# Performance work log

Hardware: AMD Instinct MI355X
Metric: run time of the kernel (lower is better)

## Reference

```python
import jax, jax.numpy as jnp
import numpy as np

N_NODES = 50000
N_EDGES = 640000
IN_CH = 64
EDGE_DIM = 16
HID = 128
OUT = 128
L = 5
N_GRAPHS = 128
BN_EPS = 1e-5


def setup_inputs() -> dict:
    key = jax.random.key(0)
    ks = jax.random.split(key, 16)

    def w(k, shape, fan_in):
        return jax.random.normal(k, shape, jnp.float32) / np.sqrt(fan_in)

    inp = {}
    inp["x"] = jax.random.normal(ks[0], (N_NODES, IN_CH), jnp.float32)
    inp["edge_index"] = jax.random.randint(ks[1], (2, N_EDGES), 0, N_NODES)
    inp["edge_attr"] = jax.random.normal(ks[2], (N_EDGES, EDGE_DIM), jnp.float32)
    inp["batch"] = jnp.sort(jax.random.randint(ks[3], (N_NODES,), 0, N_GRAPHS))
    # node / edge encoders
    inp["node_w"] = w(ks[4], (IN_CH, HID), IN_CH)
    inp["node_b"] = jnp.zeros((HID,), jnp.float32)
    inp["edge_w"] = w(ks[5], (EDGE_DIM, HID), EDGE_DIM)
    inp["edge_b"] = jnp.zeros((HID,), jnp.float32)
    # per-layer GINEConv params (stacked over L layers)
    inp["eps"] = jnp.zeros((L,), jnp.float32)  # train_eps init 0
    inp["lin_w"] = w(ks[6], (L, HID, HID), HID)       # GINEConv internal edge lin
    inp["lin_b"] = jnp.zeros((L, HID), jnp.float32)
    inp["mlp1_w"] = w(ks[7], (L, HID, 2 * HID), HID)
    inp["mlp1_b"] = jnp.zeros((L, 2 * HID), jnp.float32)
    inp["mlp2_w"] = w(ks[8], (L, 2 * HID, HID), 2 * HID)
    inp["mlp2_b"] = jnp.zeros((L, HID), jnp.float32)
    inp["bn_g"] = jnp.ones((L, HID), jnp.float32)
    inp["bn_b"] = jnp.zeros((L, HID), jnp.float32)
    # output MLP: HID -> HID//2 -> OUT
    inp["out_w1"] = w(ks[9], (HID, HID // 2), HID)
    inp["out_b1"] = jnp.zeros((HID // 2,), jnp.float32)
    inp["out_w2"] = w(ks[10], (HID // 2, OUT), HID // 2)
    inp["out_b2"] = jnp.zeros((OUT,), jnp.float32)
    return inp


def reference(x, edge_index, edge_attr, batch, node_w, node_b, edge_w, edge_b,
              eps, lin_w, lin_b, mlp1_w, mlp1_b, mlp2_w, mlp2_b, bn_g, bn_b,
              out_w1, out_b1, out_w2, out_b2):
    n_nodes = x.shape[0]
    src, dst = edge_index[0], edge_index[1]
    # node / edge encoders (dropout is identity in eval)
    h = jax.nn.relu(x @ node_w + node_b)            # [N, H]
    e = edge_attr @ edge_w + edge_b                  # [E, H]
    n_layers = lin_w.shape[0]
    for l in range(n_layers):
        # GINEConv: message = relu(x_src + lin(edge_emb)); aggregate = scatter-sum to dst
        m = jax.nn.relu(h[src] + e @ lin_w[l] + lin_b[l])      # [E, H]
        agg = jax.ops.segment_sum(m, dst, num_segments=n_nodes)  # [N, H]
        z = (1.0 + eps[l]) * h + agg
        # GINE MLP: H -> 2H -> H
        z = jax.nn.relu(z @ mlp1_w[l] + mlp1_b[l]) @ mlp2_w[l] + mlp2_b[l]
        # BatchNorm over nodes (training-mode batch statistics)
        mu = z.mean(axis=0)
        var = z.var(axis=0)
        z = (z - mu) * jax.lax.rsqrt(var + BN_EPS) * bn_g[l] + bn_b[l]
        # residual then relu
        h = jax.nn.relu(z + h)
    # global mean pool per graph
    counts = jax.ops.segment_sum(jnp.ones((n_nodes,), h.dtype), batch, num_segments=N_GRAPHS)
    pooled = jax.ops.segment_sum(h, batch, num_segments=N_GRAPHS) / jnp.maximum(counts, 1.0)[:, None]
    # output MLP (dropout identity in eval)
    logits = jax.nn.relu(pooled @ out_w1 + out_b1) @ out_w2 + out_b2
    return (logits, pooled)
```

## Files before the change

### kernel.cpp

```cpp
#include <hip/hip_runtime.h>

#define N_NODES  50000
#define NPAD     50048
#define N_EDGES  640000
#define IN_CH    64
#define EDGE_DIM 16
#define HID      128
#define HID2     256
#define NLAYER   5
#define NGRAPH   128
#define MT64     (NPAD / 64)

typedef unsigned short ushort_t;
typedef __attribute__((ext_vector_type(8))) short short8;
typedef __attribute__((ext_vector_type(4))) short s16x4;
typedef __attribute__((ext_vector_type(4))) float f32x4;
typedef __attribute__((ext_vector_type(2))) float f32x2;

__device__ __forceinline__ float b2f(ushort_t u) {
    union { unsigned v; float f; } x; x.v = ((unsigned)u) << 16; return x.f;
}
__device__ __forceinline__ ushort_t f2b(float f) {
    union { float f; unsigned u; } x; x.f = f;
    unsigned u = x.u;
    unsigned r = (u + 0x7FFFu + ((u >> 16) & 1u)) >> 16;
    return (ushort_t)r;
}

__global__ void k_transpose_cvt(const float* __restrict__ src, ushort_t* __restrict__ dst,
                                int B, int K, int Nn) {
    long total = (long)B * K * Nn;
    for (long i = (long)blockIdx.x * blockDim.x + threadIdx.x; i < total;
         i += (long)gridDim.x * blockDim.x) {
        int b = (int)(i / ((long)K * Nn));
        int rem = (int)(i - (long)b * K * Nn);
        int k = rem / Nn;
        int n = rem - k * Nn;
        dst[(long)b * K * Nn + (long)n * K + k] = f2b(src[i]);
    }
}

__global__ __launch_bounds__(128) void k_combine(const float* __restrict__ ew,
                                                 const float* __restrict__ eb,
                                                 const float* __restrict__ lw,
                                                 const float* __restrict__ lb,
                                                 ushort_t* __restrict__ WcbT,
                                                 float* __restrict__ cc) {
    int l = blockIdx.x, j = threadIdx.x;
    float accW[EDGE_DIM];
#pragma unroll
    for (int k = 0; k < EDGE_DIM; ++k) accW[k] = 0.f;
    float accc = 0.f;
    for (int i = 0; i < HID; ++i) {
        float lwv = lw[((long)l * HID + i) * HID + j];
        accc = fmaf(eb[i], lwv, accc);
#pragma unroll
        for (int k = 0; k < EDGE_DIM; ++k)
            accW[k] = fmaf(ew[k * HID + i], lwv, accW[k]);
    }
    ushort_t* wp = WcbT + ((long)l * HID + j) * 32;
#pragma unroll
    for (int k = 0; k < EDGE_DIM; ++k) wp[k] = f2b(accW[k]);
#pragma unroll
    for (int k = EDGE_DIM; k < 32; ++k) wp[k] = 0;
    cc[l * HID + j] = accc + lb[l * HID + j];
}

__global__ __launch_bounds__(256) void k_hist(const int* __restrict__ ei, int* __restrict__ deg) {
    int e = blockIdx.x * 256 + threadIdx.x;
    if (e < N_EDGES) atomicAdd(&deg[ei[N_EDGES + e]], 1);
}

__global__ __launch_bounds__(1024) void k_scan1(const int* __restrict__ deg,
                                                int* __restrict__ offs, int* __restrict__ bsum) {
    __shared__ int s[1024];
    int i = blockIdx.x * 1024 + threadIdx.x;
    int v = (i < N_NODES) ? deg[i] : 0;
    s[threadIdx.x] = v;
    __syncthreads();
    for (int off = 1; off < 1024; off <<= 1) {
        int t = (threadIdx.x >= off) ? s[threadIdx.x - off] : 0;
        __syncthreads();
        s[threadIdx.x] += t;
        __syncthreads();
    }
    if (i < N_NODES) offs[i] = s[threadIdx.x] - v;
    if (threadIdx.x == 1023) bsum[blockIdx.x] = s[1023];
}

__global__ void k_scan2(int* __restrict__ bsum, int nb) {
    if (threadIdx.x == 0 && blockIdx.x == 0) {
        int acc = 0;
        for (int i = 0; i < nb; ++i) { int v = bsum[i]; bsum[i] = acc; acc += v; }
    }
}

__global__ __launch_bounds__(1024) void k_scan3(int* __restrict__ offs, const int* __restrict__ bsum) {
    int i = blockIdx.x * 1024 + threadIdx.x;
    if (i < N_NODES) offs[i] += bsum[blockIdx.x];
}

__global__ __launch_bounds__(256) void k_scatter1(const int* __restrict__ ei,
                                                  const int* __restrict__ offs,
                                                  int* __restrict__ cursor,
                                                  int* __restrict__ perm) {
    int e = blockIdx.x * 256 + threadIdx.x;
    if (e >= N_EDGES) return;
    int d = ei[N_EDGES + e];
    int pos = offs[d] + atomicAdd(&cursor[d], 1);
    perm[pos] = e;
}

__global__ __launch_bounds__(256) void k_gather(const int* __restrict__ perm,
                                                const int* __restrict__ ei,
                                                const float* __restrict__ ea,
                                                int* __restrict__ src_s,
                                                ushort_t* __restrict__ ea_sb) {
    int p = blockIdx.x * 256 + threadIdx.x;
    if (p >= N_EDGES) return;
    int e = perm[p];
    src_s[p] = ei[e];
    const f32x4* srcp = (const f32x4*)(ea + (long)e * EDGE_DIM);
    f32x4 v0 = srcp[0], v1 = srcp[1], v2 = srcp[2], v3 = srcp[3];
    short8 o0, o1;
#pragma unroll
    for (int j = 0; j < 4; ++j) {
        o0[j] = (short)f2b(v0[j]); o0[4 + j] = (short)f2b(v1[j]);
        o1[j] = (short)f2b(v2[j]); o1[4 + j] = (short)f2b(v3[j]);
    }
    short8* dst = (short8*)(ea_sb + (long)p * EDGE_DIM);
    dst[0] = o0;
    dst[1] = o1;
}

__global__ __launch_bounds__(256) void k_node_enc(const float* __restrict__ x,
                                                  const ushort_t* __restrict__ w0T,
                                                  const float* __restrict__ nb,
                                                  float* __restrict__ h,
                                                  ushort_t* __restrict__ hb) {
    __shared__ __align__(16) short lB[HID * IN_CH];
    for (int c = threadIdx.x; c < HID * IN_CH / 8; c += 256) {
        int row = c >> 3, k0 = (c & 7) * 8;
        short8 v = *(const short8*)(w0T + row * IN_CH + k0);
        int g = (k0 >> 3) ^ (row & 7);
        *(short8*)&lB[row * IN_CH + g * 8] = v;
    }
    __syncthreads();
    int wv = threadIdx.x >> 6, l6 = threadIdx.x & 63;
    int lr = l6 & 15, lg = l6 >> 4;
    int grow = blockIdx.x * 64 + wv * 16 + lr;
    f32x4 acc[8];
#pragma unroll
    for (int nt = 0; nt < 8; ++nt) acc[nt] = (f32x4){0.f, 0.f, 0.f, 0.f};
#pragma unroll
    for (int kt = 0; kt < 2; ++kt) {
        int kk = kt * 32 + lg * 8;
        short8 a = {0, 0, 0, 0, 0, 0, 0, 0};
        if (grow < N_NODES) {
            const float* xr = x + (long)grow * IN_CH + kk;
            f32x4 v0 = *(const f32x4*)xr;
            f32x4 v1 = *(const f32x4*)(xr + 4);
#pragma unroll
            for (int j = 0; j < 4; ++j) { a[j] = (short)f2b(v0[j]); a[4 + j] = (short)f2b(v1[j]); }
        }
#pragma unroll
        for (int nt = 0; nt < 8; ++nt) {
            int brow = nt * 16 + lr;
            short8 b = *(const short8*)&lB[brow * IN_CH + (((kk >> 3) ^ (brow & 7)) << 3)];
            acc[nt] = __builtin_amdgcn_mfma_f32_16x16x32_bf16(a, b, acc[nt], 0, 0, 0);
        }
    }
    int orow0 = blockIdx.x * 64 + wv * 16 + lg * 4;
#pragma unroll
    for (int nt = 0; nt < 8; ++nt) {
        int col = nt * 16 + lr;
        float bias = nb[col];
#pragma unroll
        for (int r = 0; r < 4; ++r) {
            int row = orow0 + r;
            if (row < N_NODES) {
                float v = fmaxf(acc[nt][r] + bias, 0.f);
                h[(long)row * HID + col] = v;
                hb[(long)row * HID + col] = f2b(v);
            }
        }
    }
}

__global__ __launch_bounds__(256) void k_edgegemm(const ushort_t* __restrict__ ea_sb,
                                                  const ushort_t* __restrict__ WcbT,
                                                  const float* __restrict__ cc,
                                                  ushort_t* __restrict__ g, int l,
                                                  int ce0, int ce1) {
    int wv = threadIdx.x >> 6, l6 = threadIdx.x & 63;
    int lr = l6 & 15, lg = l6 >> 4;
    short8 af[8];
    f32x4 cv[8];
    const ushort_t* wp = WcbT + (long)l * HID * 32;
#pragma unroll
    for (int nt = 0; nt < 8; ++nt) {
        af[nt] = *(const short8*)(wp + (nt * 16 + lr) * 32 + lg * 8);
        cv[nt] = *(const f32x4*)(cc + l * HID + nt * 16 + lg * 4);
    }
    for (int it = 0; it < 4; ++it) {
        int e0 = ce0 + blockIdx.x * 256 + wv * 64 + it * 16;
        int e = e0 + lr;
        short8 b = {0, 0, 0, 0, 0, 0, 0, 0};
        if (e < ce1 && lg < 2) b = *(const short8*)(ea_sb + (long)e * EDGE_DIM + lg * 8);
        f32x4 acc[8];
#pragma unroll
        for (int nt = 0; nt < 8; ++nt) acc[nt] = (f32x4){0.f, 0.f, 0.f, 0.f};
#pragma unroll
        for (int nt = 0; nt < 8; ++nt)
            acc[nt] = __builtin_amdgcn_mfma_f32_16x16x32_bf16(af[nt], b, acc[nt], 0, 0, 0);
        if (e < ce1) {
            ushort_t* gp = g + (long)(e - ce0) * HID + lg * 4;
#pragma unroll
            for (int nt = 0; nt < 8; ++nt) {
                s16x4 o;
#pragma unroll
                for (int r = 0; r < 4; ++r) o[r] = (short)f2b(acc[nt][r] + cv[nt][r]);
                *(s16x4*)(gp + nt * 16) = o;
            }
        }
    }
}

__global__ __launch_bounds__(256) void k_edge2(const ushort_t* __restrict__ g,
                                               const int* __restrict__ src_s,
                                               const int* __restrict__ offs,
                                               const int* __restrict__ deg,
                                               const float* __restrict__ h,
                                               const ushort_t* __restrict__ hb,
                                               const float* __restrict__ epsv,
                                               float* __restrict__ zacc,
                                               ushort_t* __restrict__ z,
                                               int l, int ce0, int ce1, int mode) {
    int lane = threadIdx.x & 63;
    int node = blockIdx.x * 4 + (threadIdx.x >> 6);
    if (node >= N_NODES) return;
    bool first = mode & 1, last = (mode & 2) != 0;
    int ch0 = lane * 2;
    int s0 = offs[node];
    int dg = deg[node];
    int e_lo = max(s0, ce0);
    int e_hi = min(s0 + dg, ce1);
    if (e_lo >= e_hi && !first && !last) return;
    float a0 = 0.f, a1 = 0.f;
    int i = e_lo;
    for (; i + 4 <= e_hi; i += 4) {
        long eg = (long)(i - ce0);
        int sa = src_s[i], sb_ = src_s[i + 1], sc_ = src_s[i + 2], sd_ = src_s[i + 3];
        unsigned ga = *(const unsigned*)(g + eg * HID + ch0);
        unsigned gb = *(const unsigned*)(g + (eg + 1) * HID + ch0);
        unsigned gc = *(const unsigned*)(g + (eg + 2) * HID + ch0);
        unsigned gd = *(const unsigned*)(g + (eg + 3) * HID + ch0);
        unsigned ha = *(const unsigned*)(hb + (long)sa * HID + ch0);
        unsigned hbv = *(const unsigned*)(hb + (long)sb_ * HID + ch0);
        unsigned hc = *(const unsigned*)(hb + (long)sc_ * HID + ch0);
        unsigned hd = *(const unsigned*)(hb + (long)sd_ * HID + ch0);
        a0 += fmaxf(b2f((ushort_t)(ha & 0xffff)) + b2f((ushort_t)(ga & 0xffff)), 0.f);
        a1 += fmaxf(b2f((ushort_t)(ha >> 16)) + b2f((ushort_t)(ga >> 16)), 0.f);
        a0 += fmaxf(b2f((ushort_t)(hbv & 0xffff)) + b2f((ushort_t)(gb & 0xffff)), 0.f);
        a1 += fmaxf(b2f((ushort_t)(hbv >> 16)) + b2f((ushort_t)(gb >> 16)), 0.f);
        a0 += fmaxf(b2f((ushort_t)(hc & 0xffff)) + b2f((ushort_t)(gc & 0xffff)), 0.f);
        a1 += fmaxf(b2f((ushort_t)(hc >> 16)) + b2f((ushort_t)(gc >> 16)), 0.f);
        a0 += fmaxf(b2f((ushort_t)(hd & 0xffff)) + b2f((ushort_t)(gd & 0xffff)), 0.f);
        a1 += fmaxf(b2f((ushort_t)(hd >> 16)) + b2f((ushort_t)(gd >> 16)), 0.f);
    }
    for (; i < e_hi; ++i) {
        long eg = (long)(i - ce0);
        int s = src_s[i];
        unsigned gv = *(const unsigned*)(g + eg * HID + ch0);
        unsigned hv = *(const unsigned*)(hb + (long)s * HID + ch0);
        a0 += fmaxf(b2f((ushort_t)(hv & 0xffff)) + b2f((ushort_t)(gv & 0xffff)), 0.f);
        a1 += fmaxf(b2f((ushort_t)(hv >> 16)) + b2f((ushort_t)(gv >> 16)), 0.f);
    }
    if (!first) {
        f32x2 p = *(const f32x2*)(zacc + (long)node * HID + ch0);
        a0 += p[0]; a1 += p[1];
    }
    if (last) {
        float ep1 = 1.f + epsv[l];
        f32x2 hn = *(const f32x2*)(h + (long)node * HID + ch0);
        unsigned zz = (unsigned)f2b(fmaf(ep1, hn[0], a0)) |
                      ((unsigned)f2b(fmaf(ep1, hn[1], a1)) << 16);
        *(unsigned*)(z + (long)node * HID + ch0) = zz;
    } else {
        *(f32x2*)(zacc + (long)node * HID + ch0) = (f32x2){a0, a1};
    }
}

__global__ __launch_bounds__(256) void k_mlp1(const ushort_t* __restrict__ z,
                                              const ushort_t* __restrict__ w1T,
                                              const float* __restrict__ b1,
                                              ushort_t* __restrict__ ibuf, int l) {
    __shared__ __align__(16) short lBw[128 * HID];
    int half = blockIdx.x & 1;
    int tile = blockIdx.x >> 1;
    const ushort_t* wl = w1T + (long)l * HID2 * HID + (long)half * 128 * HID;
    for (int c = threadIdx.x; c < 128 * HID / 8; c += 256) {
        int row = c >> 4, k0 = (c & 15) * 8;
        short8 v = *(const short8*)(wl + row * HID + k0);
        int gsw = (k0 >> 3) ^ (row & 7);
        *(short8*)&lBw[row * HID + gsw * 8] = v;
    }
    int wv = threadIdx.x >> 6, l6 = threadIdx.x & 63;
    int lr = l6 & 15, lg = l6 >> 4;
    int node = tile * 64 + wv * 16 + lr;
    short8 b[4];
    const ushort_t* zr = z + (long)node * HID;
#pragma unroll
    for (int kt = 0; kt < 4; ++kt) b[kt] = *(const short8*)(zr + kt * 32 + lg * 8);
    __syncthreads();
#pragma unroll
    for (int nt = 0; nt < 8; ++nt) {
        f32x4 acc = (f32x4){0.f, 0.f, 0.f, 0.f};
        int brow = nt * 16 + lr;
#pragma unroll
        for (int kt = 0; kt < 4; ++kt) {
            short8 af = *(const short8*)&lBw[brow * HID + (((kt * 4 + lg) ^ (brow & 7)) << 3)];
            acc = __builtin_amdgcn_mfma_f32_16x16x32_bf16(af, b[kt], acc, 0, 0, 0);
        }
        f32x4 bv = *(const f32x4*)(b1 + l * HID2 + half * 128 + nt * 16 + lg * 4);
        s16x4 o;
#pragma unroll
        for (int r = 0; r < 4; ++r) o[r] = (short)f2b(fmaxf(acc[r] + bv[r], 0.f));
        *(s16x4*)(ibuf + (long)node * HID2 + half * 128 + nt * 16 + lg * 4) = o;
    }
}

__global__ __launch_bounds__(256) void k_mlp2(const ushort_t* __restrict__ ibuf,
                                              const ushort_t* __restrict__ w2T,
                                              const float* __restrict__ b2,
                                              ushort_t* __restrict__ z2,
                                              float* __restrict__ bnstats, int l) {
    __shared__ __align__(16) short lBw[64 * HID2];
    __shared__ float lStat[2][64];
    int half = blockIdx.x & 1;
    int tile = blockIdx.x >> 1;
    const ushort_t* wl = w2T + (long)l * HID * HID2 + (long)half * 64 * HID2;
    for (int c = threadIdx.x; c < 64 * HID2 / 8; c += 256) {
        int row = c >> 5, k0 = (c & 31) * 8;
        short8 v = *(const short8*)(wl + row * HID2 + k0);
        int gsw = (k0 >> 3) ^ (row & 7);
        *(short8*)&lBw[row * HID2 + gsw * 8] = v;
    }
    if (threadIdx.x < 128) lStat[threadIdx.x >> 6][threadIdx.x & 63] = 0.f;
    int wv = threadIdx.x >> 6, l6 = threadIdx.x & 63;
    int lr = l6 & 15, lg = l6 >> 4;
    int node = tile * 64 + wv * 16 + lr;
    bool valid = node < N_NODES;
    short8 b[8];
    const ushort_t* ir = ibuf + (long)node * HID2;
#pragma unroll
    for (int kt = 0; kt < 8; ++kt) b[kt] = *(const short8*)(ir + kt * 32 + lg * 8);
    __syncthreads();
#pragma unroll
    for (int nt = 0; nt < 4; ++nt) {
        f32x4 acc = (f32x4){0.f, 0.f, 0.f, 0.f};
        int brow = nt * 16 + lr;
#pragma unroll
        for (int kt = 0; kt < 8; ++kt) {
            short8 af = *(const short8*)&lBw[brow * HID2 + (((kt * 4 + lg) ^ (brow & 7)) << 3)];
            acc = __builtin_amdgcn_mfma_f32_16x16x32_bf16(af, b[kt], acc, 0, 0, 0);
        }
        f32x4 bv = *(const f32x4*)(b2 + l * HID + half * 64 + nt * 16 + lg * 4);
        s16x4 o;
#pragma unroll
        for (int r = 0; r < 4; ++r) {
            float v = acc[r] + bv[r];
            o[r] = (short)f2b(v);
            float s = valid ? v : 0.f, q = valid ? v * v : 0.f;
            s += __shfl_xor(s, 1); s += __shfl_xor(s, 2);
            s += __shfl_xor(s, 4); s += __shfl_xor(s, 8);
            q += __shfl_xor(q, 1); q += __shfl_xor(q, 2);
            q += __shfl_xor(q, 4); q += __shfl_xor(q, 8);
            if (lr == 0) {
                int f = nt * 16 + lg * 4 + r;
                atomicAdd(&lStat[0][f], s);
                atomicAdd(&lStat[1][f], q);
            }
        }
        *(s16x4*)(z2 + (long)node * HID + half * 64 + nt * 16 + lg * 4) = o;
    }
    __syncthreads();
    if (threadIdx.x < 128) {
        int which = threadIdx.x >> 6, f = threadIdx.x & 63;
        atomicAdd(&bnstats[(which * NLAYER + l) * HID + half * 64 + f], lStat[which][f]);
    }
}

__global__ __launch_bounds__(1024) void k_resid(const ushort_t* __restrict__ z2,
                                                const float* __restrict__ bnstats,
                                                const float* __restrict__ bng,
                                                const float* __restrict__ bnb,
                                                float* __restrict__ h,
                                                ushort_t* __restrict__ hb, int l) {
    long i = (long)blockIdx.x * 1024 + threadIdx.x;
    int c = (int)(i & (HID - 1));
    float inv = 1.f / (float)N_NODES;
    float mu = bnstats[l * HID + c] * inv;
    float var = bnstats[(NLAYER + l) * HID + c] * inv - mu * mu;
    float A = rsqrtf(var + 1e-5f) * bng[l * HID + c];
    float B = bnb[l * HID + c] - mu * A;
    float v = fmaf(b2f(z2[i]), A, B) + h[i];
    v = fmaxf(v, 0.f);
    h[i] = v;
    hb[i] = f2b(v);
}

__global__ void k_gstart(const int* __restrict__ batch, int* __restrict__ gstart) {
    int g = threadIdx.x;
    if (g > NGRAPH) return;
    int lo = 0, hi = N_NODES;
    while (lo < hi) { int mid = (lo + hi) >> 1; if (batch[mid] < g) lo = mid + 1; else hi = mid; }
    gstart[g] = lo;
}

__global__ __launch_bounds__(512) void k_pool(const float* __restrict__ h,
                                              const int* __restrict__ gstart,
                                              float* __restrict__ pooled,
                                              float* __restrict__ outp) {
    __shared__ float red[4][HID];
    int g = blockIdx.x;
    int ch = threadIdx.x & 127, seg = threadIdx.x >> 7;
    int st = gstart[g], en = gstart[g + 1];
    float s = 0.f;
    for (int i = st + seg; i < en; i += 4) s += h[(long)i * HID + ch];
    red[seg][ch] = s;
    __syncthreads();
    if (seg == 0) {
        float p = (red[0][ch] + red[1][ch] + red[2][ch] + red[3][ch]) /
                  fmaxf((float)(en - st), 1.f);
        pooled[g * HID + ch] = p;
        outp[g * HID + ch] = p;
    }
}

__global__ __launch_bounds__(128) void k_outmlp(const float* __restrict__ pooled,
                                                const float* __restrict__ w1,
                                                const float* __restrict__ b1,
                                                const float* __restrict__ w2,
                                                const float* __restrict__ b2,
                                                float* __restrict__ outl) {
    __shared__ float pr[HID];
    __shared__ float hid[64];
    int g = blockIdx.x, t = threadIdx.x;
    pr[t] = pooled[g * HID + t];
    __syncthreads();
    if (t < 64) {
        float a = b1[t];
        for (int k = 0; k < HID; ++k) a = fmaf(pr[k], w1[k * 64 + t], a);
        hid[t] = fmaxf(a, 0.f);
    }
    __syncthreads();
    float a = b2[t];
#pragma unroll
    for (int j = 0; j < 64; ++j) a = fmaf(hid[j], w2[j * HID + t], a);
    outl[g * HID + t] = a;
}

extern "C" void kernel_launch(void* const* d_in, const int* in_sizes, int n_in,
                              void* d_out, int out_size, void* d_ws, size_t ws_size,
                              hipStream_t stream) {
    (void)in_sizes; (void)n_in; (void)out_size;
    const float* x      = (const float*)d_in[0];
    const int*   ei     = (const int*)d_in[1];
    const float* ea     = (const float*)d_in[2];
    const int*   batch  = (const int*)d_in[3];
    const float* node_w = (const float*)d_in[4];
    const float* node_b = (const float*)d_in[5];
    const float* edge_w = (const float*)d_in[6];
    const float* edge_b = (const float*)d_in[7];
    const float* epsv   = (const float*)d_in[8];
    const float* lin_w  = (const float*)d_in[9];
    const float* lin_b  = (const float*)d_in[10];
    const float* m1w    = (const float*)d_in[11];
    const float* m1b    = (const float*)d_in[12];
    const float* m2w    = (const float*)d_in[13];
    const float* m2b    = (const float*)d_in[14];
    const float* bng    = (const float*)d_in[15];
    const float* bnb    = (const float*)d_in[16];
    const float* ow1    = (const float*)d_in[17];
    const float* ob1    = (const float*)d_in[18];
    const float* ow2    = (const float*)d_in[19];
    const float* ob2    = (const float*)d_in[20];

    const size_t MiB = 1024ull * 1024ull;
    int NC;
    if      (ws_size >= 275 * MiB) NC = 1;
    else if (ws_size >= 193 * MiB) NC = 2;
    else if (ws_size >= 152 * MiB) NC = 4;
    else                           NC = 8;
    int EC = (N_EDGES + NC - 1) / NC;

    char* ws = (char*)d_ws;
    size_t off = 0;
    auto alloc = [&](size_t bytes) -> char* {
        char* p = ws + off;
        off = (off + bytes + 255) & ~(size_t)255;
        return p;
    };
    float*    h       = (float*)alloc((size_t)NPAD * HID * 4);
    ushort_t* hb      = (ushort_t*)alloc((size_t)NPAD * HID * 2);
    ushort_t* z       = (ushort_t*)alloc((size_t)NPAD * HID * 2);
    ushort_t* ibuf    = (ushort_t*)alloc((size_t)NPAD * HID2 * 2);
    ushort_t* ea_sb   = (ushort_t*)alloc((size_t)N_EDGES * EDGE_DIM * 2 + 64);
    ushort_t* g       = (ushort_t*)alloc((size_t)EC * HID * 2);
    int*      src_s   = (int*)alloc((size_t)N_EDGES * 4);
    int*      deg     = (int*)alloc((size_t)N_NODES * 4);
    int*      offs    = (int*)alloc((size_t)N_NODES * 4);
    int*      cursor  = (int*)alloc((size_t)N_NODES * 4);
    int*      bsum    = (int*)alloc(64 * 4);
    ushort_t* WcbT    = (ushort_t*)alloc((size_t)NLAYER * HID * 32 * 2);
    float*    cc      = (float*)alloc((size_t)NLAYER * HID * 4);
    ushort_t* w0T     = (ushort_t*)alloc((size_t)HID * IN_CH * 2);
    ushort_t* w1T     = (ushort_t*)alloc((size_t)NLAYER * HID2 * HID * 2);
    ushort_t* w2T     = (ushort_t*)alloc((size_t)NLAYER * HID * HID2 * 2);
    float*    bnstats = (float*)alloc((size_t)2 * NLAYER * HID * 4);
    int*      gstart  = (int*)alloc((NGRAPH + 1) * 4);
    float*    pooled  = (float*)alloc((size_t)NGRAPH * HID * 4);
    float*    zacc    = (float*)ibuf;
    int*      perm    = (int*)ibuf;
    ushort_t* z2      = z;

    (void)hipMemsetAsync(deg, 0, (size_t)N_NODES * 4, stream);
    (void)hipMemsetAsync(cursor, 0, (size_t)N_NODES * 4, stream);
    (void)hipMemsetAsync(bnstats, 0, (size_t)2 * NLAYER * HID * 4, stream);

    k_transpose_cvt<<<64, 256, 0, stream>>>(node_w, w0T, 1, IN_CH, HID);
    k_transpose_cvt<<<640, 256, 0, stream>>>(m1w, w1T, NLAYER, HID, HID2);
    k_transpose_cvt<<<640, 256, 0, stream>>>(m2w, w2T, NLAYER, HID2, HID);
    k_combine<<<NLAYER, HID, 0, stream>>>(edge_w, edge_b, lin_w, lin_b, WcbT, cc);

    k_hist<<<N_EDGES / 256, 256, 0, stream>>>(ei, deg);
    k_scan1<<<49, 1024, 0, stream>>>(deg, offs, bsum);
    k_scan2<<<1, 1, 0, stream>>>(bsum, 49);
    k_scan3<<<49, 1024, 0, stream>>>(offs, bsum);
    k_scatter1<<<N_EDGES / 256, 256, 0, stream>>>(ei, offs, cursor, perm);
    k_gather<<<N_EDGES / 256, 256, 0, stream>>>(perm, ei, ea, src_s, ea_sb);

    k_node_enc<<<NPAD / 64, 256, 0, stream>>>(x, w0T, node_b, h, hb);

    for (int l = 0; l < NLAYER; ++l) {
        for (int c = 0; c < NC; ++c) {
            int ce0 = c * EC;
            int ce1 = (ce0 + EC < N_EDGES) ? (ce0 + EC) : N_EDGES;
            int nblk = (ce1 - ce0 + 255) / 256;
            int mode = (c == 0 ? 1 : 0) | (c == NC - 1 ? 2 : 0);
            k_edgegemm<<<nblk, 256, 0, stream>>>(ea_sb, WcbT, cc, g, l, ce0, ce1);
            k_edge2<<<(N_NODES + 3) / 4, 256, 0, stream>>>(g, src_s, offs, deg, h, hb,
                                                           epsv, zacc, z, l, ce0, ce1, mode);
        }
        k_mlp1<<<MT64 * 2, 256, 0, stream>>>(z, w1T, m1b, ibuf, l);
        k_mlp2<<<MT64 * 2, 256, 0, stream>>>(ibuf, w2T, m2b, z2, bnstats, l);
        k_resid<<<(N_NODES * HID) / 1024, 1024, 0, stream>>>(z2, bnstats, bng, bnb, h, hb, l);
    }

    k_gstart<<<1, 256, 0, stream>>>(batch, gstart);
    k_pool<<<NGRAPH, 512, 0, stream>>>(h, gstart, pooled, (float*)d_out + NGRAPH * HID);
    k_outmlp<<<NGRAPH, HID, 0, stream>>>(pooled, ow1, ob1, ow2, ob2, (float*)d_out);
}
```

Before: 1.090 ms.

## Merge setup kernels, parallelize block-sum scan, fold gstart into pool, widen edge2 blocks

```diff
diff --git a/kernel.cpp b/kernel.cpp
--- a/kernel.cpp
+++ b/kernel.cpp
@@ -27,16 +27,34 @@
     return (ushort_t)r;
 }
 
-__global__ void k_transpose_cvt(const float* __restrict__ src, ushort_t* __restrict__ dst,
-                                int B, int K, int Nn) {
-    long total = (long)B * K * Nn;
+__global__ void k_transpose_all(const float* __restrict__ w0,
+                                const float* __restrict__ w1,
+                                const float* __restrict__ w2,
+                                ushort_t* __restrict__ w0T,
+                                ushort_t* __restrict__ w1T,
+                                ushort_t* __restrict__ w2T) {
+    const long n0 = (long)IN_CH * HID;
+    const long n1 = (long)NLAYER * HID * HID2;
+    const long n2 = (long)NLAYER * HID2 * HID;
+    long total = n0 + n1 + n2;
     for (long i = (long)blockIdx.x * blockDim.x + threadIdx.x; i < total;
          i += (long)gridDim.x * blockDim.x) {
-        int b = (int)(i / ((long)K * Nn));
-        int rem = (int)(i - (long)b * K * Nn);
-        int k = rem / Nn;
-        int n = rem - k * Nn;
-        dst[(long)b * K * Nn + (long)n * K + k] = f2b(src[i]);
+        if (i < n0) {
+            int k = (int)(i / HID), n = (int)(i - (long)k * HID);
+            w0T[(long)n * IN_CH + k] = f2b(w0[i]);
+        } else if (i < n0 + n1) {
+            long j = i - n0;
+            int b = (int)(j / ((long)HID * HID2));
+            int rem = (int)(j - (long)b * HID * HID2);
+            int k = rem / HID2, n = rem - k * HID2;
+            w1T[(long)b * HID * HID2 + (long)n * HID + k] = f2b(w1[j]);
+        } else {
+            long j = i - n0 - n1;
+            int b = (int)(j / ((long)HID2 * HID));
+            int rem = (int)(j - (long)b * HID2 * HID);
+            int k = rem / HID, n = rem - k * HID;
+            w2T[(long)b * HID2 * HID + (long)n * HID2 + k] = f2b(w2[j]);
+        }
     }
 }
 
@@ -89,10 +107,15 @@
 }
 
 __global__ void k_scan2(int* __restrict__ bsum, int nb) {
-    if (threadIdx.x == 0 && blockIdx.x == 0) {
-        int acc = 0;
-        for (int i = 0; i < nb; ++i) { int v = bsum[i]; bsum[i] = acc; acc += v; }
-    }
+    int t = threadIdx.x;
+    int v = (t < nb) ? bsum[t] : 0;
+    int x = v;
+#pragma unroll
+    for (int off = 1; off < 64; off <<= 1) {
+        int y = __shfl_up(x, off);
+        if ((t & 63) >= off) x += y;
+    }
+    if (t < nb) bsum[t] = x - v;
 }
 
 __global__ __launch_bounds__(1024) void k_scan3(int* __restrict__ offs, const int* __restrict__ bsum) {
@@ -226,7 +249,7 @@
     }
 }
 
-__global__ __launch_bounds__(256) void k_edge2(const ushort_t* __restrict__ g,
+__global__ __launch_bounds__(512) void k_edge2(const ushort_t* __restrict__ g,
                                                const int* __restrict__ src_s,
                                                const int* __restrict__ offs,
                                                const int* __restrict__ deg,
@@ -237,7 +260,7 @@
                                                ushort_t* __restrict__ z,
                                                int l, int ce0, int ce1, int mode) {
     int lane = threadIdx.x & 63;
-    int node = blockIdx.x * 4 + (threadIdx.x >> 6);
+    int node = blockIdx.x * 8 + (threadIdx.x >> 6);
     if (node >= N_NODES) return;
     bool first = mode & 1, last = (mode & 2) != 0;
     int ch0 = lane * 2;
@@ -410,22 +433,22 @@
     hb[i] = f2b(v);
 }
 
-__global__ void k_gstart(const int* __restrict__ batch, int* __restrict__ gstart) {
-    int g = threadIdx.x;
-    if (g > NGRAPH) return;
-    int lo = 0, hi = N_NODES;
-    while (lo < hi) { int mid = (lo + hi) >> 1; if (batch[mid] < g) lo = mid + 1; else hi = mid; }
-    gstart[g] = lo;
-}
-
 __global__ __launch_bounds__(512) void k_pool(const float* __restrict__ h,
-                                              const int* __restrict__ gstart,
+                                              const int* __restrict__ batch,
                                               float* __restrict__ pooled,
                                               float* __restrict__ outp) {
     __shared__ float red[4][HID];
+    __shared__ int sb[2];
     int g = blockIdx.x;
+    if (threadIdx.x < 2) {
+        int target = g + threadIdx.x;
+        int lo = 0, hi = N_NODES;
+        while (lo < hi) { int mid = (lo + hi) >> 1; if (batch[mid] < target) lo = mid + 1; else hi = mid; }
+        sb[threadIdx.x] = lo;
+    }
+    __syncthreads();
+    int st = sb[0], en = sb[1];
     int ch = threadIdx.x & 127, seg = threadIdx.x >> 7;
-    int st = gstart[g], en = gstart[g + 1];
     float s = 0.f;
     for (int i = st + seg; i < en; i += 4) s += h[(long)i * HID + ch];
     red[seg][ch] = s;
@@ -519,7 +542,6 @@
     ushort_t* w1T     = (ushort_t*)alloc((size_t)NLAYER * HID2 * HID * 2);
     ushort_t* w2T     = (ushort_t*)alloc((size_t)NLAYER * HID * HID2 * 2);
     float*    bnstats = (float*)alloc((size_t)2 * NLAYER * HID * 4);
-    int*      gstart  = (int*)alloc((NGRAPH + 1) * 4);
     float*    pooled  = (float*)alloc((size_t)NGRAPH * HID * 4);
     float*    zacc    = (float*)ibuf;
     int*      perm    = (int*)ibuf;
@@ -529,14 +551,12 @@
     (void)hipMemsetAsync(cursor, 0, (size_t)N_NODES * 4, stream);
     (void)hipMemsetAsync(bnstats, 0, (size_t)2 * NLAYER * HID * 4, stream);
 
-    k_transpose_cvt<<<64, 256, 0, stream>>>(node_w, w0T, 1, IN_CH, HID);
-    k_transpose_cvt<<<640, 256, 0, stream>>>(m1w, w1T, NLAYER, HID, HID2);
-    k_transpose_cvt<<<640, 256, 0, stream>>>(m2w, w2T, NLAYER, HID2, HID);
+    k_transpose_all<<<1280, 256, 0, stream>>>(node_w, m1w, m2w, w0T, w1T, w2T);
     k_combine<<<NLAYER, HID, 0, stream>>>(edge_w, edge_b, lin_w, lin_b, WcbT, cc);
 
     k_hist<<<N_EDGES / 256, 256, 0, stream>>>(ei, deg);
     k_scan1<<<49, 1024, 0, stream>>>(deg, offs, bsum);
-    k_scan2<<<1, 1, 0, stream>>>(bsum, 49);
+    k_scan2<<<1, 64, 0, stream>>>(bsum, 49);
     k_scan3<<<49, 1024, 0, stream>>>(offs, bsum);
     k_scatter1<<<N_EDGES / 256, 256, 0, stream>>>(ei, offs, cursor, perm);
     k_gather<<<N_EDGES / 256, 256, 0, stream>>>(perm, ei, ea, src_s, ea_sb);
@@ -550,7 +570,7 @@
             int nblk = (ce1 - ce0 + 255) / 256;
             int mode = (c == 0 ? 1 : 0) | (c == NC - 1 ? 2 : 0);
             k_edgegemm<<<nblk, 256, 0, stream>>>(ea_sb, WcbT, cc, g, l, ce0, ce1);
-            k_edge2<<<(N_NODES + 3) / 4, 256, 0, stream>>>(g, src_s, offs, deg, h, hb,
+            k_edge2<<<(N_NODES + 7) / 8, 512, 0, stream>>>(g, src_s, offs, deg, h, hb,
                                                            epsv, zacc, z, l, ce0, ce1, mode);
         }
         k_mlp1<<<MT64 * 2, 256, 0, stream>>>(z, w1T, m1b, ibuf, l);
@@ -558,7 +578,6 @@
         k_resid<<<(N_NODES * HID) / 1024, 1024, 0, stream>>>(z2, bnstats, bng, bnb, h, hb, l);
     }
 
-    k_gstart<<<1, 256, 0, stream>>>(batch, gstart);
-    k_pool<<<NGRAPH, 512, 0, stream>>>(h, gstart, pooled, (float*)d_out + NGRAPH * HID);
+    k_pool<<<NGRAPH, 512, 0, stream>>>(h, batch, pooled, (float*)d_out + NGRAPH * HID);
     k_outmlp<<<NGRAPH, HID, 0, stream>>>(pooled, ow1, ob1, ow2, ob2, (float*)d_out);
 }
```

Result: no change. 1.078 ms (-1.1%).
